# Performance work log

Measured on AMD Instinct MI355X. Metric: run time of the kernel, lower is better.

## Reference

```python
import jax, jax.numpy as jnp
import numpy as np

N = 50000
NEG_SLOPE = 0.2  # PyG GATConv default negative_slope


def gat_conv(x, src, dst, W, a_src, a_dst, b, num_nodes):
    """PyG-style GATConv (concat=True, add_self_loops handled by caller).
    x: [N, Fin], src/dst: [E'] (self-loops included), W: [Fin, H*C],
    a_src/a_dst: [H, C], b: [H*C].
    """
    H, C = a_src.shape
    h = (x @ W).reshape(num_nodes, H, C)                      # [N, H, C]
    alpha_src = jnp.einsum('nhc,hc->nh', h, a_src)            # [N, H]
    alpha_dst = jnp.einsum('nhc,hc->nh', h, a_dst)            # [N, H]
    e = jax.nn.leaky_relu(alpha_src[src] + alpha_dst[dst], NEG_SLOPE)  # [E', H]
    # segment softmax over edges grouped by destination node
    m = jax.ops.segment_max(e, dst, num_segments=num_nodes)   # [N, H]
    m = jnp.where(jnp.isfinite(m), m, 0.0)
    ex = jnp.exp(e - m[dst])                                  # [E', H]
    denom = jax.ops.segment_sum(ex, dst, num_segments=num_nodes)
    alpha = ex / (denom[dst] + 1e-16)                          # [E', H]
    # weighted scatter-sum of source features to destinations
    out = jax.ops.segment_sum(alpha[:, :, None] * h[src], dst, num_segments=num_nodes)
    return out.reshape(num_nodes, H * C) + b


def setup_inputs() -> dict:
    key = jax.random.key(0)
    ks = jax.random.split(key, 10)
    Fin, Hid, Out, Hds = 128, 32, 64, 4
    E = 800000
    x = jax.random.normal(ks[0], (N, Fin), dtype=jnp.float32)
    edge_index = jax.random.randint(ks[1], (2, E), 0, N, dtype=jnp.int64)
    s1 = (1.0 / np.sqrt(Fin)).astype(np.float32) if isinstance(np.sqrt(Fin), np.ndarray) else np.float32(1.0 / np.sqrt(Fin))
    s2 = np.float32(1.0 / np.sqrt(Hid * Hds))
    return {
        'x': x,
        'edge_index': edge_index,
        'W1': jax.random.normal(ks[2], (Fin, Hds * Hid), dtype=jnp.float32) * s1,
        'att_src1': jax.random.normal(ks[3], (Hds, Hid), dtype=jnp.float32) * 0.1,
        'att_dst1': jax.random.normal(ks[4], (Hds, Hid), dtype=jnp.float32) * 0.1,
        'b1': jnp.zeros((Hds * Hid,), dtype=jnp.float32),
        'W2': jax.random.normal(ks[5], (Hds * Hid, Out), dtype=jnp.float32) * s2,
        'att_src2': jax.random.normal(ks[6], (1, Out), dtype=jnp.float32) * 0.1,
        'att_dst2': jax.random.normal(ks[7], (1, Out), dtype=jnp.float32) * 0.1,
        'b2': jnp.zeros((Out,), dtype=jnp.float32),
    }


def reference(x, edge_index, W1, att_src1, att_dst1, b1, W2, att_src2, att_dst2, b2):
    num_nodes = x.shape[0]
    loop = jnp.arange(num_nodes, dtype=edge_index.dtype)
    src = jnp.concatenate([edge_index[0], loop])  # add self-loops (PyG default)
    dst = jnp.concatenate([edge_index[1], loop])
    h = gat_conv(x, src, dst, W1, att_src1, att_dst1, b1, num_nodes)
    h = jax.nn.relu(h)
    out = gat_conv(h, src, dst, W2, att_src2, att_dst2, b2, num_nodes)
    return out
```

## Files before the change

kernel.cpp:

```cpp
#include <hip/hip_runtime.h>
#include <hip/hip_fp16.h>

#define NN 50000
#define EE 800000
#define ELL (EE + NN)
#define NSLICE 8
#define SLICE_W (NN / NSLICE)


__global__ void detect_kernel(const unsigned* __restrict__ ei_words,
                              int* __restrict__ flag) {
  if (threadIdx.x == 0 && blockIdx.x == 0) {
    unsigned acc = 0;
    for (int i = 1; i < 64; i += 2) acc |= ei_words[i];
    *flag = (acc == 0u) ? 1 : 0;
  }
}

__device__ __forceinline__ int edge_at(const void* ei, int is64, long long idx) {
  if (is64) return (int)((const long long*)ei)[idx];
  return ((const int*)ei)[idx];
}


__global__ void __launch_bounds__(256) zero_kernel(int* __restrict__ p, int n) {
  int stride = gridDim.x * blockDim.x;
  for (int i = blockIdx.x * blockDim.x + threadIdx.x; i < n; i += stride) p[i] = 0;
}

__global__ void __launch_bounds__(256) count_kernel(const void* __restrict__ ei,
                                                    const int* __restrict__ flag,
                                                    int* __restrict__ cnt) {
  int is64 = *flag;
  int fam = blockIdx.x & (NSLICE - 1);
  int bf = blockIdx.x >> 3;
  int nf = gridDim.x >> 3;
  int lo = fam * SLICE_W, hi = lo + SLICE_W;
  for (int i = bf * blockDim.x + threadIdx.x; i < ELL; i += nf * blockDim.x) {
    int d = (i < EE) ? edge_at(ei, is64, (long long)EE + i) : (i - EE);
    if (d >= lo && d < hi) atomicAdd(&cnt[d], 1);
  }
}

__global__ void __launch_bounds__(256) scan1_kernel(const int* __restrict__ cnt,
                                                    int* __restrict__ excl,
                                                    int* __restrict__ bsum) {
  __shared__ int sh[256];
  int t = threadIdx.x;
  int base = blockIdx.x * 1024 + t * 4;
  int v0 = 0, v1 = 0, v2 = 0, v3 = 0;
  if (base + 0 < NN) v0 = cnt[base + 0];
  if (base + 1 < NN) v1 = cnt[base + 1];
  if (base + 2 < NN) v2 = cnt[base + 2];
  if (base + 3 < NN) v3 = cnt[base + 3];
  int s = v0 + v1 + v2 + v3;
  sh[t] = s;
  __syncthreads();
  for (int off = 1; off < 256; off <<= 1) {
    int x = (t >= off) ? sh[t - off] : 0;
    __syncthreads();
    sh[t] += x;
    __syncthreads();
  }
  if (t == 255) bsum[blockIdx.x] = sh[255];
  int run = sh[t] - s;
  if (base + 0 < NN) excl[base + 0] = run;
  run += v0;
  if (base + 1 < NN) excl[base + 1] = run;
  run += v1;
  if (base + 2 < NN) excl[base + 2] = run;
  run += v2;
  if (base + 3 < NN) excl[base + 3] = run;
}

__global__ void scan2_kernel(int* __restrict__ bsum, int nb) {
  if (threadIdx.x == 0 && blockIdx.x == 0) {
    int run = 0;
    for (int i = 0; i < nb; ++i) { int x = bsum[i]; bsum[i] = run; run += x; }
    bsum[nb] = run;
  }
}

__global__ void __launch_bounds__(256) scan3_kernel(int* __restrict__ row_ptr,
                                                    const int* __restrict__ bsum,
                                                    int nb) {
  int i = blockIdx.x * blockDim.x + threadIdx.x;
  if (i < NN) row_ptr[i] += bsum[i >> 10];
  if (i == 0) row_ptr[NN] = bsum[nb];
}

__global__ void __launch_bounds__(256) scatter_kernel(const void* __restrict__ ei,
                                                      const int* __restrict__ flag,
                                                      const int* __restrict__ row_ptr,
                                                      int* __restrict__ cursor,
                                                      int* __restrict__ srcs_sorted) {
  int is64 = *flag;
  int fam = blockIdx.x & (NSLICE - 1);
  int bf = blockIdx.x >> 3;
  int nf = gridDim.x >> 3;
  int lo = fam * SLICE_W, hi = lo + SLICE_W;
  for (int i = bf * blockDim.x + threadIdx.x; i < ELL; i += nf * blockDim.x) {
    int s, d;
    if (i < EE) {
      s = edge_at(ei, is64, i);
      d = edge_at(ei, is64, (long long)EE + i);
    } else {
      s = d = i - EE;
    }
    if (d < lo || d >= hi || (unsigned)s >= (unsigned)NN) continue;
    int pos = row_ptr[d] + atomicAdd(&cursor[d], 1);
    if ((unsigned)pos < (unsigned)ELL) srcs_sorted[pos] = s;
  }
}


template <int BM, int BN, int BK, int TM, int TN, int AMODE>
__global__ void __launch_bounds__(256) gemm_alpha(const float* __restrict__ A,
                                                  const float* __restrict__ B,
                                                  __half* __restrict__ C,
                                                  const float* __restrict__ a_srcv,
                                                  const float* __restrict__ a_dstv,
                                                  float* __restrict__ asrc_out,
                                                  float* __restrict__ adst_out,
                                                  int M, int N, int K) {
  constexpr int THREADS = (BM / TM) * (BN / TN);
  static_assert(THREADS == 256, "block must be 256 threads");
  static_assert(BM * BK == 1024, "A tile = 4 floats/thread");
  static_assert((TN % 4) == 0 && (TM % 4) == 0, "microtile shape");
  constexpr int BPT = (BK * BN) / THREADS;
  static_assert(BPT == 2 || BPT == 4, "B tile load width");
  __shared__ float As[BK][BM + 4];
  __shared__ float Bs[BK][BN + 4];
  int tid = threadIdx.x;
  int tx = tid % (BN / TN);
  int ty = tid / (BN / TN);
  int row0 = blockIdx.x * BM;
  int col0 = blockIdx.y * BN;
  float acc[TM][TN] = {};
  for (int k0 = 0; k0 < K; k0 += BK) {
    {
      int m = tid / (BK / 4);
      int kk = (tid % (BK / 4)) * 4;
      float4 v = make_float4(0.f, 0.f, 0.f, 0.f);
      int gr = row0 + m;
      if (gr < M) v = *(const float4*)&A[(size_t)gr * K + k0 + kk];
      As[kk + 0][m] = v.x; As[kk + 1][m] = v.y;
      As[kk + 2][m] = v.z; As[kk + 3][m] = v.w;
    }
    if constexpr (BPT == 4) {
      constexpr int T_PER_ROW = BN / 4;
      int kr = tid / T_PER_ROW;
      int nc = (tid % T_PER_ROW) * 4;
      *(float4*)&Bs[kr][nc] = *(const float4*)&B[(size_t)(k0 + kr) * N + col0 + nc];
    } else {
      constexpr int T_PER_ROW = BN / 2;
      int kr = tid / T_PER_ROW;
      int nc = (tid % T_PER_ROW) * 2;
      *(float2*)&Bs[kr][nc] = *(const float2*)&B[(size_t)(k0 + kr) * N + col0 + nc];
    }
    __syncthreads();
    #pragma unroll
    for (int k = 0; k < BK; ++k) {
      float a[TM], b[TN];
      #pragma unroll
      for (int i = 0; i < TM; i += 4)
        *(float4*)&a[i] = *(const float4*)&As[k][ty * TM + i];
      #pragma unroll
      for (int j = 0; j < TN; j += 4)
        *(float4*)&b[j] = *(const float4*)&Bs[k][tx * TN + j];
      #pragma unroll
      for (int i = 0; i < TM; ++i)
        #pragma unroll
        for (int j = 0; j < TN; ++j) acc[i][j] += a[i] * b[j];
    }
    __syncthreads();
  }
  #pragma unroll
  for (int i = 0; i < TM; ++i) {
    int gr = row0 + ty * TM + i;
    if (gr >= M) continue;
    __half tmp[TN];
    #pragma unroll
    for (int j = 0; j < TN; ++j) tmp[j] = __float2half(acc[i][j]);
    if constexpr (TN == 8)
      *(float4*)&C[(size_t)gr * N + col0 + tx * TN] = *(float4*)tmp;
    else
      *(float2*)&C[(size_t)gr * N + col0 + tx * TN] = *(float2*)tmp;
  }
  if (AMODE == 1) {
    int hh = tx >> 2;
    int co = (tx & 3) * TN;
    #pragma unroll
    for (int i = 0; i < TM; ++i) {
      float sA = 0.f, sD = 0.f;
      #pragma unroll
      for (int j = 0; j < TN; ++j) {
        float v = acc[i][j];
        sA += v * a_srcv[hh * 32 + co + j];
        sD += v * a_dstv[hh * 32 + co + j];
      }
      sA += __shfl_xor(sA, 1, 64); sA += __shfl_xor(sA, 2, 64);
      sD += __shfl_xor(sD, 1, 64); sD += __shfl_xor(sD, 2, 64);
      int gr = row0 + ty * TM + i;
      if ((tx & 3) == 0 && gr < M) {
        asrc_out[gr * 4 + hh] = sA;
        adst_out[gr * 4 + hh] = sD;
      }
    }
  } else if (AMODE == 2) {
    #pragma unroll
    for (int i = 0; i < TM; ++i) {
      float sA = 0.f, sD = 0.f;
      #pragma unroll
      for (int j = 0; j < TN; ++j) {
        float v = acc[i][j];
        sA += v * a_srcv[tx * TN + j];
        sD += v * a_dstv[tx * TN + j];
      }
      #pragma unroll
      for (int m = 1; m <= 8; m <<= 1) {
        sA += __shfl_xor(sA, m, 64);
        sD += __shfl_xor(sD, m, 64);
      }
      int gr = row0 + ty * TM + i;
      if (tx == 0 && gr < M) { asrc_out[gr] = sA; adst_out[gr] = sD; }
    }
  }
}


__device__ __forceinline__ float leaky(float x) { return x > 0.f ? x : 0.2f * x; }

__global__ void __launch_bounds__(256) agg1_fused(
    const __half* __restrict__ h,
    const int* __restrict__ row_ptr,
    const int* __restrict__ srcs,
    const float* __restrict__ asrc,
    const float* __restrict__ adst,
    const float* __restrict__ b1,
    float* __restrict__ out)
{
  int lane = threadIdx.x & 63;
  int grp = lane >> 5;
  int cl = lane & 31;
  int c0 = cl * 4;
  int myh = cl >> 3;
  int wid = (blockIdx.x * blockDim.x + threadIdx.x) >> 6;
  int nw = (gridDim.x * blockDim.x) >> 6;
  float4 bb = *(const float4*)&b1[c0];
  for (int n = wid; n < NN; n += nw) {
    int rbeg = row_ptr[n], rend = row_ptr[n + 1];
    float ad = adst[n * 4 + myh];
    float dsum = grp ? 0.f : 1e-16f;
    float a0 = 0.f, a1 = 0.f, a2 = 0.f, a3 = 0.f;
    #pragma unroll 2
    for (int e = rbeg + grp; e < rend; e += 2) {
      int s = srcs[e];
      float wgt = __expf(leaky(asrc[s * 4 + myh] + ad));
      float2 raw = *(const float2*)&h[(size_t)s * 128 + c0];
      float2 f01 = __half22float2(__builtin_bit_cast(__half2, raw.x));
      float2 f23 = __half22float2(__builtin_bit_cast(__half2, raw.y));
      dsum += wgt;
      a0 += wgt * f01.x; a1 += wgt * f01.y;
      a2 += wgt * f23.x; a3 += wgt * f23.y;
    }
    dsum += __shfl_xor(dsum, 32, 64);
    a0 += __shfl_xor(a0, 32, 64);
    a1 += __shfl_xor(a1, 32, 64);
    a2 += __shfl_xor(a2, 32, 64);
    a3 += __shfl_xor(a3, 32, 64);
    if (lane < 32) {
      float inv = 1.f / dsum;
      float4 o = make_float4(fmaxf(a0 * inv + bb.x, 0.f),
                             fmaxf(a1 * inv + bb.y, 0.f),
                             fmaxf(a2 * inv + bb.z, 0.f),
                             fmaxf(a3 * inv + bb.w, 0.f));
      *(float4*)&out[(size_t)n * 128 + c0] = o;
    }
  }
}

__global__ void __launch_bounds__(256) agg2_kernel(
    const __half* __restrict__ h,
    const int* __restrict__ row_ptr,
    const int* __restrict__ srcs,
    const float* __restrict__ asrc,
    const float* __restrict__ adst,
    const float* __restrict__ b2,
    float* __restrict__ out)
{
  int lane = threadIdx.x & 63;
  int grp = lane >> 4;
  int cl = lane & 15;
  int c0 = cl * 4;
  int wid = (blockIdx.x * blockDim.x + threadIdx.x) >> 6;
  int nw = (gridDim.x * blockDim.x) >> 6;
  float4 bb = *(const float4*)&b2[c0];
  for (int n = wid; n < NN; n += nw) {
    int rbeg = row_ptr[n], rend = row_ptr[n + 1];
    float ad = adst[n];
    float dsum = (grp == 0) ? 1e-16f : 0.f;
    float a0 = 0.f, a1 = 0.f, a2 = 0.f, a3 = 0.f;
    #pragma unroll 2
    for (int e = rbeg + grp; e < rend; e += 4) {
      int s = srcs[e];
      float wgt = __expf(leaky(asrc[s] + ad));
      float2 raw = *(const float2*)&h[(size_t)s * 64 + c0];
      float2 f01 = __half22float2(__builtin_bit_cast(__half2, raw.x));
      float2 f23 = __half22float2(__builtin_bit_cast(__half2, raw.y));
      dsum += wgt;
      a0 += wgt * f01.x; a1 += wgt * f01.y;
      a2 += wgt * f23.x; a3 += wgt * f23.y;
    }
    #pragma unroll
    for (int m = 16; m <= 32; m <<= 1) {
      dsum += __shfl_xor(dsum, m, 64);
      a0 += __shfl_xor(a0, m, 64);
      a1 += __shfl_xor(a1, m, 64);
      a2 += __shfl_xor(a2, m, 64);
      a3 += __shfl_xor(a3, m, 64);
    }
    if (lane < 16) {
      float inv = 1.f / dsum;
      float4 o = make_float4(a0 * inv + bb.x, a1 * inv + bb.y,
                             a2 * inv + bb.z, a3 * inv + bb.w);
      *(float4*)&out[(size_t)n * 64 + c0] = o;
    }
  }
}


extern "C" void kernel_launch(void* const* d_in, const int* in_sizes, int n_in,
                              void* d_out, int out_size, void* d_ws, size_t ws_size,
                              hipStream_t stream) {
  const float* x   = (const float*)d_in[0];
  const void*  ei  = d_in[1];
  const float* W1  = (const float*)d_in[2];
  const float* as1 = (const float*)d_in[3];
  const float* ad1 = (const float*)d_in[4];
  const float* b1  = (const float*)d_in[5];
  const float* W2  = (const float*)d_in[6];
  const float* as2 = (const float*)d_in[7];
  const float* ad2 = (const float*)d_in[8];
  const float* b2  = (const float*)d_in[9];
  float* out = (float*)d_out;

  char* w = (char*)d_ws;
  __half* h1h  = (__half*)w; w += (size_t)NN * 128 * 2;
  __half* hb2h = h1h;
  float* h2    = (float*)w; w += (size_t)NN * 128 * 4;
  float* asrc1 = (float*)w; w += (size_t)NN * 4 * 4;
  float* adst1 = (float*)w; w += (size_t)NN * 4 * 4;
  float* asrc2 = (float*)w; w += (size_t)NN * 4;
  float* adst2 = (float*)w; w += (size_t)NN * 4;
  int* cnt     = (int*)w;   w += (size_t)NN * 4;
  int* cursor  = (int*)w;   w += (size_t)NN * 4;
  int* row_ptr = (int*)w;   w += (size_t)(NN + 1) * 4;
  int* bsum    = (int*)w;   w += 256;
  int* is64    = (int*)w;   w += 256;
  int* srcs_sorted = (int*)w; w += (size_t)ELL * 4;

  const int NB = (NN + 1023) / 1024;

  detect_kernel<<<1, 64, 0, stream>>>((const unsigned*)ei, is64);
  zero_kernel<<<256, 256, 0, stream>>>(cnt, 2 * NN);
  count_kernel<<<2048, 256, 0, stream>>>(ei, is64, cnt);
  scan1_kernel<<<NB, 256, 0, stream>>>(cnt, row_ptr, bsum);
  scan2_kernel<<<1, 64, 0, stream>>>(bsum, NB);
  scan3_kernel<<<(NN + 255) / 256, 256, 0, stream>>>(row_ptr, bsum, NB);
  scatter_kernel<<<2048, 256, 0, stream>>>(ei, is64, row_ptr, cursor, srcs_sorted);

  const int MB128 = (NN + 127) / 128;

  gemm_alpha<128, 128, 8, 8, 8, 1><<<dim3(MB128, 1), 256, 0, stream>>>(
      x, W1, h1h, as1, ad1, asrc1, adst1, NN, 128, 128);
  agg1_fused<<<4096, 256, 0, stream>>>(h1h, row_ptr, srcs_sorted, asrc1, adst1, b1, h2);

  gemm_alpha<128, 64, 8, 8, 4, 2><<<dim3(MB128, 1), 256, 0, stream>>>(
      h2, W2, hb2h, as2, ad2, asrc2, adst2, NN, 64, 128);
  agg2_kernel<<<4096, 256, 0, stream>>>(hb2h, row_ptr, srcs_sorted, asrc2, adst2, b2, out);
}
```

Measured before the change: 216.0 us.

## Precompute layer-1 edge weights during CSR scatter and merge detect into zero kernel

Moves the scatter kernel after the first GEMM so it can compute the per-edge, per-head unnormalized attention weights exp(leaky(asrc+adst)) and store them as fp16 in CSR order. agg1 then reads these weights contiguously instead of gathering asrc per source and evaluating exp in the inner loop. The detect and zero kernels are fused into one launch, and the aggregation loops are unrolled 4 instead of 2. The cost is an extra ELL*4 fp16 buffer written with scattered stores, fp16 rounding of the exp weights, and scatter now carrying a random gather of asrc.

```diff
diff --git a/kernel.cpp b/kernel.cpp
--- a/kernel.cpp
+++ b/kernel.cpp
@@ -7,26 +7,26 @@
 #define NSLICE 8
 #define SLICE_W (NN / NSLICE)
 
-
-__global__ void detect_kernel(const unsigned* __restrict__ ei_words,
-                              int* __restrict__ flag) {
-  if (threadIdx.x == 0 && blockIdx.x == 0) {
+__device__ __forceinline__ int edge_at(const void* ei, int is64, long long idx) {
+  if (is64) return (int)((const long long*)ei)[idx];
+  return ((const int*)ei)[idx];
+}
+
+__device__ __forceinline__ float leaky(float x) { return x > 0.f ? x : 0.2f * x; }
+
+
+__global__ void __launch_bounds__(256) zero_detect_kernel(int* __restrict__ p, int n,
+                                                          const unsigned* __restrict__ ei_words,
+                                                          int* __restrict__ flag) {
+  if (blockIdx.x == 0 && threadIdx.x == 0) {
     unsigned acc = 0;
     for (int i = 1; i < 64; i += 2) acc |= ei_words[i];
     *flag = (acc == 0u) ? 1 : 0;
   }
-}
-
-__device__ __forceinline__ int edge_at(const void* ei, int is64, long long idx) {
-  if (is64) return (int)((const long long*)ei)[idx];
-  return ((const int*)ei)[idx];
-}
-
-
-__global__ void __launch_bounds__(256) zero_kernel(int* __restrict__ p, int n) {
   int stride = gridDim.x * blockDim.x;
   for (int i = blockIdx.x * blockDim.x + threadIdx.x; i < n; i += stride) p[i] = 0;
 }
+
 
 __global__ void __launch_bounds__(256) count_kernel(const void* __restrict__ ei,
                                                     const int* __restrict__ flag,
@@ -93,7 +93,10 @@
                                                       const int* __restrict__ flag,
                                                       const int* __restrict__ row_ptr,
                                                       int* __restrict__ cursor,
-                                                      int* __restrict__ srcs_sorted) {
+                                                      int* __restrict__ srcs_sorted,
+                                                      const float* __restrict__ asrc,
+                                                      const float* __restrict__ adst,
+                                                      __half* __restrict__ w1h) {
   int is64 = *flag;
   int fam = blockIdx.x & (NSLICE - 1);
   int bf = blockIdx.x >> 3;
@@ -109,7 +112,17 @@
     }
     if (d < lo || d >= hi || (unsigned)s >= (unsigned)NN) continue;
     int pos = row_ptr[d] + atomicAdd(&cursor[d], 1);
-    if ((unsigned)pos < (unsigned)ELL) srcs_sorted[pos] = s;
+    if ((unsigned)pos < (unsigned)ELL) {
+      srcs_sorted[pos] = s;
+      float4 as4 = *(const float4*)&asrc[s * 4];
+      float4 ad4 = *(const float4*)&adst[d * 4];
+      __half hw[4];
+      hw[0] = __float2half(__expf(leaky(as4.x + ad4.x)));
+      hw[1] = __float2half(__expf(leaky(as4.y + ad4.y)));
+      hw[2] = __float2half(__expf(leaky(as4.z + ad4.z)));
+      hw[3] = __float2half(__expf(leaky(as4.w + ad4.w)));
+      *(uint2*)&w1h[(size_t)pos * 4] = *(uint2*)hw;
+    }
   }
 }
 
@@ -229,14 +242,11 @@
 }
 
 
-__device__ __forceinline__ float leaky(float x) { return x > 0.f ? x : 0.2f * x; }
-
 __global__ void __launch_bounds__(256) agg1_fused(
     const __half* __restrict__ h,
     const int* __restrict__ row_ptr,
     const int* __restrict__ srcs,
-    const float* __restrict__ asrc,
-    const float* __restrict__ adst,
+    const __half* __restrict__ w1h,
     const float* __restrict__ b1,
     float* __restrict__ out)
 {
@@ -250,13 +260,15 @@
   float4 bb = *(const float4*)&b1[c0];
   for (int n = wid; n < NN; n += nw) {
     int rbeg = row_ptr[n], rend = row_ptr[n + 1];
-    float ad = adst[n * 4 + myh];
     float dsum = grp ? 0.f : 1e-16f;
     float a0 = 0.f, a1 = 0.f, a2 = 0.f, a3 = 0.f;
-    #pragma unroll 2
+    #pragma unroll 4
     for (int e = rbeg + grp; e < rend; e += 2) {
       int s = srcs[e];
-      float wgt = __expf(leaky(asrc[s * 4 + myh] + ad));
+      uint2 wraw = *(const uint2*)&w1h[(size_t)e * 4];
+      unsigned wsel = (myh & 2) ? wraw.y : wraw.x;
+      __half2 hw = __builtin_bit_cast(__half2, wsel);
+      float wgt = (myh & 1) ? __high2float(hw) : __low2float(hw);
       float2 raw = *(const float2*)&h[(size_t)s * 128 + c0];
       float2 f01 = __half22float2(__builtin_bit_cast(__half2, raw.x));
       float2 f23 = __half22float2(__builtin_bit_cast(__half2, raw.y));
@@ -301,7 +313,7 @@
     float ad = adst[n];
     float dsum = (grp == 0) ? 1e-16f : 0.f;
     float a0 = 0.f, a1 = 0.f, a2 = 0.f, a3 = 0.f;
-    #pragma unroll 2
+    #pragma unroll 4
     for (int e = rbeg + grp; e < rend; e += 4) {
       int s = srcs[e];
       float wgt = __expf(leaky(asrc[s] + ad));
@@ -359,22 +371,24 @@
   int* bsum    = (int*)w;   w += 256;
   int* is64    = (int*)w;   w += 256;
   int* srcs_sorted = (int*)w; w += (size_t)ELL * 4;
+  __half* w1h  = (__half*)w; w += (size_t)ELL * 4 * 2;
 
   const int NB = (NN + 1023) / 1024;
-
-  detect_kernel<<<1, 64, 0, stream>>>((const unsigned*)ei, is64);
-  zero_kernel<<<256, 256, 0, stream>>>(cnt, 2 * NN);
+  const int MB128 = (NN + 127) / 128;
+
+  zero_detect_kernel<<<256, 256, 0, stream>>>(cnt, 2 * NN, (const unsigned*)ei, is64);
   count_kernel<<<2048, 256, 0, stream>>>(ei, is64, cnt);
   scan1_kernel<<<NB, 256, 0, stream>>>(cnt, row_ptr, bsum);
   scan2_kernel<<<1, 64, 0, stream>>>(bsum, NB);
   scan3_kernel<<<(NN + 255) / 256, 256, 0, stream>>>(row_ptr, bsum, NB);
-  scatter_kernel<<<2048, 256, 0, stream>>>(ei, is64, row_ptr, cursor, srcs_sorted);
-
-  const int MB128 = (NN + 127) / 128;
 
   gemm_alpha<128, 128, 8, 8, 8, 1><<<dim3(MB128, 1), 256, 0, stream>>>(
       x, W1, h1h, as1, ad1, asrc1, adst1, NN, 128, 128);
-  agg1_fused<<<4096, 256, 0, stream>>>(h1h, row_ptr, srcs_sorted, asrc1, adst1, b1, h2);
+
+  scatter_kernel<<<2048, 256, 0, stream>>>(ei, is64, row_ptr, cursor, srcs_sorted,
+                                           asrc1, adst1, w1h);
+
+  agg1_fused<<<4096, 256, 0, stream>>>(h1h, row_ptr, srcs_sorted, w1h, b1, h2);
 
   gemm_alpha<128, 64, 8, 8, 4, 2><<<dim3(MB128, 1), 256, 0, stream>>>(
       h2, W2, hb2h, as2, ad2, asrc2, adst2, NN, 64, 128);
```

New measurement: 218.3 us. About the same (+1.1%).
